# Performance work log

Measured on AMD Instinct MI355X. Metric: run time of the kernel, lower is better.

Reference implementation:

```python
import jax, jax.numpy as jnp
import numpy as np

N_ENTITIES = 200_000
N_RELATIONS = 2
EMBED_DIM = 64
N_EDGES = 2_000_000


def setup_inputs() -> dict:
    key = jax.random.key(0)
    k1, k2, k3, k4, k5, k6, k7, k8 = jax.random.split(key, 8)
    edge_index = jax.random.randint(k1, (2, N_EDGES), 0, N_ENTITIES, dtype=jnp.int32)
    edge_type = jax.random.randint(k2, (N_EDGES,), 0, N_RELATIONS, dtype=jnp.int32)
    entity_emb = jax.random.normal(k3, (N_ENTITIES, EMBED_DIM), dtype=jnp.float32)
    relation_emb = jax.random.normal(k4, (N_RELATIONS, EMBED_DIM), dtype=jnp.float32)
    att_w = jax.random.normal(k5, (2 * EMBED_DIM, 1), dtype=jnp.float32) * 0.08
    att_b = jax.random.normal(k6, (1,), dtype=jnp.float32) * 0.08
    W_w = jax.random.normal(k7, (EMBED_DIM, EMBED_DIM), dtype=jnp.float32) * 0.12
    W_b = jax.random.normal(k8, (EMBED_DIM,), dtype=jnp.float32) * 0.12
    return {
        "edge_index": edge_index,
        "edge_type": edge_type,
        "entity_emb": entity_emb,
        "relation_emb": relation_emb,
        "att_w": att_w,
        "att_b": att_b,
        "W_w": W_w,
        "W_b": W_b,
    }


def reference(edge_index, edge_type, entity_emb, relation_emb, att_w, att_b, W_w, W_b):
    # Gather per-edge embeddings: [E, D]
    head = entity_emb[edge_index[0]]
    tail = entity_emb[edge_index[1]]
    rel = relation_emb[edge_type]
    # Attention score per edge: sigmoid(Linear(cat(head, rel)))  -> [E, 1]
    head_rel = jnp.concatenate([head, rel], axis=-1)
    att_scores = jax.nn.sigmoid(head_rel @ att_w + att_b)
    # Weighted messages and scatter-add into head nodes (the Python loop in the
    # original is exactly a segment_sum over head indices).
    neighbor_emb = att_scores * tail  # [E, D]
    aggr_emb = jax.ops.segment_sum(neighbor_emb, edge_index[0], num_segments=N_ENTITIES)
    # Final transform: tanh(W @ aggr + b)
    return jnp.tanh(aggr_emb @ W_w.T + W_b)
```

## Files before the change

kernel.cpp:

```cpp
#include <hip/hip_runtime.h>
#include <hip/hip_bf16.h>


#define DIM 64
#define TMASK 0x3FFFF
#define RBIT (1 << 18)
#define BSH 8
#define NBK_MAX 800
#define CHUNK 6144
#define SCAN_ITEMS 4
#define S1_ITEMS 2

__global__ __launch_bounds__(256) void kgat_front(
    const float* __restrict__ emb, const float* __restrict__ rel,
    const float* __restrict__ att_w, const float* __restrict__ att_b,
    const int* __restrict__ ei,
    float* __restrict__ hdot, float* __restrict__ rb,
    int* __restrict__ bcnt,
    int n_ent, int n_rel, int E, int nbk, int hblocks) {
  __shared__ int hist[NBK_MAX];
  if ((int)blockIdx.x < hblocks) {
    int gid = blockIdx.x * 256 + threadIdx.x;
    int n = gid >> 4;
    int q = threadIdx.x & 15;
    if (n >= n_ent + n_rel) return;
    float4 v, w;
    if (n < n_ent) {
      v = ((const float4*)emb)[n * 16 + q];
      w = ((const float4*)att_w)[q];
    } else {
      v = ((const float4*)rel)[(n - n_ent) * 16 + q];
      w = ((const float4*)att_w)[16 + q];
    }
    float p = v.x * w.x + v.y * w.y + v.z * w.z + v.w * w.w;
    p += __shfl_xor(p, 1);
    p += __shfl_xor(p, 2);
    p += __shfl_xor(p, 4);
    p += __shfl_xor(p, 8);
    if (q == 0) {
      if (n < n_ent) hdot[n] = p;
      else rb[n - n_ent] = p + att_b[0];
    }
  } else {
    for (int i = threadIdx.x; i < NBK_MAX; i += 256) hist[i] = 0;
    __syncthreads();
    int base = ((int)blockIdx.x - hblocks) * CHUNK;
    for (int i = threadIdx.x; i < CHUNK; i += 256) {
      int e = base + i;
      if (e < E) atomicAdd(&hist[ei[e] >> BSH], 1);
    }
    __syncthreads();
    for (int b = threadIdx.x; b < nbk; b += 256) {
      int c = hist[b];
      if (c) atomicAdd(&bcnt[b << 4], c);
    }
  }
}

__global__ __launch_bounds__(256) void kgat_bscan(
    const int* __restrict__ bcnt, int* __restrict__ boff,
    int* __restrict__ gcur, int nbk) {
  __shared__ int sblk[256];
  int v[SCAN_ITEMS];
  int s = 0;
#pragma unroll
  for (int k = 0; k < SCAN_ITEMS; ++k) {
    int idx = threadIdx.x * SCAN_ITEMS + k;
    v[k] = (idx < nbk) ? bcnt[idx << 4] : 0;
    s += v[k];
  }
  sblk[threadIdx.x] = s;
  __syncthreads();
  for (int d = 1; d < 256; d <<= 1) {
    int t = (threadIdx.x >= (unsigned)d) ? sblk[threadIdx.x - d] : 0;
    __syncthreads();
    sblk[threadIdx.x] += t;
    __syncthreads();
  }
  int excl = sblk[threadIdx.x] - s;
#pragma unroll
  for (int k = 0; k < SCAN_ITEMS; ++k) {
    int idx = threadIdx.x * SCAN_ITEMS + k;
    if (idx < nbk) {
      boff[idx] = excl;
      gcur[idx << 4] = excl;
    }
    excl += v[k];
  }
  if (threadIdx.x == 255) boff[nbk] = excl;
}

__global__ __launch_bounds__(512) void kgat_scatter1(
    const int* __restrict__ ei, const int* __restrict__ et,
    int* __restrict__ gcur, int* __restrict__ stage, int E, int nbk) {
  __shared__ int hist[NBK_MAX];
  __shared__ int lstart[NBK_MAX];
  __shared__ int lcur[NBK_MAX];
  __shared__ int sblk[512];
  __shared__ int vals[CHUNK];
  __shared__ unsigned short bid[CHUNK];
  int tid = threadIdx.x;
  int base = blockIdx.x * CHUNK;
  for (int i = tid; i < NBK_MAX; i += 512) hist[i] = 0;
  __syncthreads();
  for (int i = tid; i < CHUNK; i += 512) {
    int e = base + i;
    if (e < E) atomicAdd(&hist[ei[e] >> BSH], 1);
  }
  __syncthreads();
  int v[S1_ITEMS];
  int s = 0;
#pragma unroll
  for (int k = 0; k < S1_ITEMS; ++k) {
    int idx = tid * S1_ITEMS + k;
    v[k] = (idx < nbk) ? hist[idx] : 0;
    s += v[k];
  }
  sblk[tid] = s;
  __syncthreads();
  for (int d = 1; d < 512; d <<= 1) {
    int t = (tid >= d) ? sblk[tid - d] : 0;
    __syncthreads();
    sblk[tid] += t;
    __syncthreads();
  }
  int excl = sblk[tid] - s;
#pragma unroll
  for (int k = 0; k < S1_ITEMS; ++k) {
    int idx = tid * S1_ITEMS + k;
    if (idx < nbk) {
      lstart[idx] = excl;
      lcur[idx] = excl;
    }
    excl += v[k];
  }
  __syncthreads();
  for (int b = tid; b < nbk; b += 512) {
    int c = hist[b];
    hist[b] = c ? atomicAdd(&gcur[b << 4], c) : 0;
  }
  __syncthreads();
  for (int i = tid; i < CHUNK; i += 512) {
    int e = base + i;
    if (e < E) {
      int h = ei[e];
      int t = ei[E + e];
      int r = et[e];
      int b = h >> BSH;
      int pos = atomicAdd(&lcur[b], 1);
      vals[pos] = t | (r << 18) | ((h & 255) << 19);
      bid[pos] = (unsigned short)b;
    }
  }
  __syncthreads();
  int cc = E - base;
  if (cc > CHUNK) cc = CHUNK;
  for (int p = tid; p < cc; p += 512) {
    int b = bid[p];
    stage[hist[b] + (p - lstart[b])] = vals[p];
  }
}

__global__ __launch_bounds__(256) void kgat_scatter2(
    const int* __restrict__ stage, const int* __restrict__ boff,
    int* __restrict__ off, int* __restrict__ payload) {
  __shared__ int hist[256];
  __shared__ int sc[256];
  __shared__ int lcur[256];
  int b = blockIdx.x;
  int tid = threadIdx.x;
  int s0 = boff[b], s1 = boff[b + 1];
  hist[tid] = 0;
  __syncthreads();
  for (int p = s0 + tid; p < s1; p += 256)
    atomicAdd(&hist[(stage[p] >> 19) & 255], 1);
  __syncthreads();
  int c = hist[tid];
  sc[tid] = c;
  __syncthreads();
  for (int d = 1; d < 256; d <<= 1) {
    int t = (tid >= d) ? sc[tid - d] : 0;
    __syncthreads();
    sc[tid] += t;
    __syncthreads();
  }
  int basep = s0 + sc[tid] - c;
  off[(b << 8) + tid] = basep;
  lcur[tid] = basep;
  __syncthreads();
  for (int p = s0 + tid; p < s1; p += 256) {
    int vv = stage[p];
    int pos = atomicAdd(&lcur[(vv >> 19) & 255], 1);
    payload[pos] = vv;
  }
}

__global__ __launch_bounds__(256) void kgat_aggr_fused(
    const int* __restrict__ off, const int* __restrict__ payload,
    const float* __restrict__ emb, const float* __restrict__ hdot,
    const float* __restrict__ rb, const float* __restrict__ Ww,
    const float* __restrict__ Wb, float* __restrict__ out, int n) {
  __shared__ float Ws[64][68];
  for (int idx = threadIdx.x; idx < 64 * 64; idx += 256) {
    int j = idx >> 6, i = idx & 63;
    Ws[i][j] = Ww[idx];
  }
  __syncthreads();
  int q = threadIdx.x & 15;
  int grp = threadIdx.x >> 4;
  int lanebase = (threadIdx.x & 63) & ~15;
  int stride = gridDim.x * 16;
  float r0 = rb[0], r1 = rb[1];
  float4 bb = ((const float4*)Wb)[q];
  const float4* emb4 = (const float4*)emb;
  for (int h = blockIdx.x * 16 + grp; h < n; h += stride) {
    int p = off[h];
    int p1 = off[h + 1];
    float hd = hdot[h];
    float sc0 = 1.0f / (1.0f + __expf(-(hd + r0)));
    float sc1 = 1.0f / (1.0f + __expf(-(hd + r1)));
    float4 acc = make_float4(0.f, 0.f, 0.f, 0.f);
    for (; p + 4 <= p1; p += 4) {
      int v0 = payload[p + 0];
      int v1 = payload[p + 1];
      int v2 = payload[p + 2];
      int v3 = payload[p + 3];
      float4 t0 = emb4[(v0 & TMASK) * 16 + q];
      float4 t1 = emb4[(v1 & TMASK) * 16 + q];
      float4 t2 = emb4[(v2 & TMASK) * 16 + q];
      float4 t3 = emb4[(v3 & TMASK) * 16 + q];
      float s0 = (v0 & RBIT) ? sc1 : sc0;
      float s1 = (v1 & RBIT) ? sc1 : sc0;
      float s2 = (v2 & RBIT) ? sc1 : sc0;
      float s3 = (v3 & RBIT) ? sc1 : sc0;
      acc.x = fmaf(s0, t0.x, acc.x); acc.y = fmaf(s0, t0.y, acc.y);
      acc.z = fmaf(s0, t0.z, acc.z); acc.w = fmaf(s0, t0.w, acc.w);
      acc.x = fmaf(s1, t1.x, acc.x); acc.y = fmaf(s1, t1.y, acc.y);
      acc.z = fmaf(s1, t1.z, acc.z); acc.w = fmaf(s1, t1.w, acc.w);
      acc.x = fmaf(s2, t2.x, acc.x); acc.y = fmaf(s2, t2.y, acc.y);
      acc.z = fmaf(s2, t2.z, acc.z); acc.w = fmaf(s2, t2.w, acc.w);
      acc.x = fmaf(s3, t3.x, acc.x); acc.y = fmaf(s3, t3.y, acc.y);
      acc.z = fmaf(s3, t3.z, acc.z); acc.w = fmaf(s3, t3.w, acc.w);
    }
    for (; p < p1; ++p) {
      int v0 = payload[p];
      float s0 = (v0 & RBIT) ? sc1 : sc0;
      float4 t0 = emb4[(v0 & TMASK) * 16 + q];
      acc.x = fmaf(s0, t0.x, acc.x); acc.y = fmaf(s0, t0.y, acc.y);
      acc.z = fmaf(s0, t0.z, acc.z); acc.w = fmaf(s0, t0.w, acc.w);
    }
    float4 o = bb;
#pragma unroll 4
    for (int j = 0; j < 16; ++j) {
      float a0 = __shfl(acc.x, lanebase + j);
      float a1 = __shfl(acc.y, lanebase + j);
      float a2 = __shfl(acc.z, lanebase + j);
      float a3 = __shfl(acc.w, lanebase + j);
      float4 w0 = *(const float4*)&Ws[4 * j + 0][4 * q];
      float4 w1 = *(const float4*)&Ws[4 * j + 1][4 * q];
      float4 w2 = *(const float4*)&Ws[4 * j + 2][4 * q];
      float4 w3 = *(const float4*)&Ws[4 * j + 3][4 * q];
      o.x = fmaf(a0, w0.x, o.x); o.y = fmaf(a0, w0.y, o.y);
      o.z = fmaf(a0, w0.z, o.z); o.w = fmaf(a0, w0.w, o.w);
      o.x = fmaf(a1, w1.x, o.x); o.y = fmaf(a1, w1.y, o.y);
      o.z = fmaf(a1, w1.z, o.z); o.w = fmaf(a1, w1.w, o.w);
      o.x = fmaf(a2, w2.x, o.x); o.y = fmaf(a2, w2.y, o.y);
      o.z = fmaf(a2, w2.z, o.z); o.w = fmaf(a2, w2.w, o.w);
      o.x = fmaf(a3, w3.x, o.x); o.y = fmaf(a3, w3.y, o.y);
      o.z = fmaf(a3, w3.z, o.z); o.w = fmaf(a3, w3.w, o.w);
    }
    o.x = tanhf(o.x); o.y = tanhf(o.y); o.z = tanhf(o.z); o.w = tanhf(o.w);
    ((float4*)out)[h * 16 + q] = o;
  }
}

extern "C" void kernel_launch(void* const* d_in, const int* in_sizes, int n_in,
                              void* d_out, int out_size, void* d_ws, size_t ws_size,
                              hipStream_t stream) {
  const int* edge_index = (const int*)d_in[0];
  const int* edge_type  = (const int*)d_in[1];
  const float* entity_emb   = (const float*)d_in[2];
  const float* relation_emb = (const float*)d_in[3];
  const float* att_w = (const float*)d_in[4];
  const float* att_b = (const float*)d_in[5];
  const float* W_w   = (const float*)d_in[6];
  const float* W_b   = (const float*)d_in[7];
  float* out = (float*)d_out;

  const int E     = in_sizes[0] / 2;
  const int N_ENT = in_sizes[2] / DIM;
  const int N_REL = in_sizes[3] / DIM;
  const int NBK   = (N_ENT + 255) >> BSH;

  int* w32 = (int*)d_ws;
  float* hdot = (float*)w32;
  float* rb   = (float*)(w32 + N_ENT);
  int*   bcnt = w32 + N_ENT + 8;
  int*   boff = bcnt + NBK * 16;
  int*   gcur = boff + NBK + 1;
  int*   off  = gcur + NBK * 16;
  int*   stage   = off + NBK * 256 + 1;
  int*   payload = stage + E;

  hipMemsetAsync(bcnt, 0, (size_t)NBK * 16 * sizeof(int), stream);

  int hblocks = ((N_ENT + N_REL) * 16 + 255) / 256;
  int eblocks = (E + CHUNK - 1) / CHUNK;
  kgat_front<<<hblocks + eblocks, 256, 0, stream>>>(
      entity_emb, relation_emb, att_w, att_b, edge_index,
      hdot, rb, bcnt, N_ENT, N_REL, E, NBK, hblocks);
  kgat_bscan<<<1, 256, 0, stream>>>(bcnt, boff, gcur, NBK);
  kgat_scatter1<<<eblocks, 512, 0, stream>>>(edge_index, edge_type, gcur, stage, E, NBK);
  kgat_scatter2<<<NBK, 256, 0, stream>>>(stage, boff, off, payload);
  kgat_aggr_fused<<<2048, 256, 0, stream>>>(off, payload, entity_emb, hdot, rb,
                                            W_w, W_b, out, N_ENT);
}
```

Before: 177.8 us.

## Fuse per-bucket counting sort into aggregation kernel using shared memory

Merges the second-level sort (scatter2) into the aggregation kernel. Each 512-thread block now sorts its 256-node bucket's edges into LDS and then aggregates and transforms those nodes directly. This removes one launch plus the global payload and offset write and read round trip. In exchange it uses a large LDS footprint (about 36KB), which may lower occupancy, and grid size shrinks to NBK (~782) blocks. There is a slow fallback path for buckets above SCAP edges.

```diff
diff --git a/kernel.cpp b/kernel.cpp
--- a/kernel.cpp
+++ b/kernel.cpp
@@ -10,6 +10,7 @@
 #define CHUNK 6144
 #define SCAN_ITEMS 4
 #define S1_ITEMS 2
+#define SCAP 4608
 
 __global__ __launch_bounds__(256) void kgat_front(
     const float* __restrict__ emb, const float* __restrict__ rel,
@@ -161,116 +162,161 @@
   }
 }
 
-__global__ __launch_bounds__(256) void kgat_scatter2(
-    const int* __restrict__ stage, const int* __restrict__ boff,
-    int* __restrict__ off, int* __restrict__ payload) {
-  __shared__ int hist[256];
-  __shared__ int sc[256];
-  __shared__ int lcur[256];
-  int b = blockIdx.x;
-  int tid = threadIdx.x;
-  int s0 = boff[b], s1 = boff[b + 1];
-  hist[tid] = 0;
-  __syncthreads();
-  for (int p = s0 + tid; p < s1; p += 256)
-    atomicAdd(&hist[(stage[p] >> 19) & 255], 1);
-  __syncthreads();
-  int c = hist[tid];
-  sc[tid] = c;
-  __syncthreads();
-  for (int d = 1; d < 256; d <<= 1) {
-    int t = (tid >= d) ? sc[tid - d] : 0;
-    __syncthreads();
-    sc[tid] += t;
-    __syncthreads();
-  }
-  int basep = s0 + sc[tid] - c;
-  off[(b << 8) + tid] = basep;
-  lcur[tid] = basep;
-  __syncthreads();
-  for (int p = s0 + tid; p < s1; p += 256) {
-    int vv = stage[p];
-    int pos = atomicAdd(&lcur[(vv >> 19) & 255], 1);
-    payload[pos] = vv;
-  }
-}
-
-__global__ __launch_bounds__(256) void kgat_aggr_fused(
-    const int* __restrict__ off, const int* __restrict__ payload,
+__global__ __launch_bounds__(512) void kgat_aggr2(
+    const int* __restrict__ boff, const int* __restrict__ stage,
     const float* __restrict__ emb, const float* __restrict__ hdot,
     const float* __restrict__ rb, const float* __restrict__ Ww,
     const float* __restrict__ Wb, float* __restrict__ out, int n) {
   __shared__ float Ws[64][68];
-  for (int idx = threadIdx.x; idx < 64 * 64; idx += 256) {
+  __shared__ int svals[SCAP];
+  __shared__ int hist[256];
+  __shared__ int sc[256];
+  __shared__ int lcur[256];
+  int tid = threadIdx.x;
+  int b = blockIdx.x;
+  for (int idx = tid; idx < 64 * 64; idx += 512) {
     int j = idx >> 6, i = idx & 63;
     Ws[i][j] = Ww[idx];
   }
-  __syncthreads();
-  int q = threadIdx.x & 15;
-  int grp = threadIdx.x >> 4;
-  int lanebase = (threadIdx.x & 63) & ~15;
-  int stride = gridDim.x * 16;
+  int q = tid & 15;
+  int grp = tid >> 4;
+  int lanebase = (tid & 63) & ~15;
+  int h0 = b << 8;
+  int s0 = boff[b], s1 = boff[b + 1];
+  int m = s1 - s0;
   float r0 = rb[0], r1 = rb[1];
-  float4 bb = ((const float4*)Wb)[q];
   const float4* emb4 = (const float4*)emb;
-  for (int h = blockIdx.x * 16 + grp; h < n; h += stride) {
-    int p = off[h];
-    int p1 = off[h + 1];
-    float hd = hdot[h];
-    float sc0 = 1.0f / (1.0f + __expf(-(hd + r0)));
-    float sc1 = 1.0f / (1.0f + __expf(-(hd + r1)));
-    float4 acc = make_float4(0.f, 0.f, 0.f, 0.f);
-    for (; p + 4 <= p1; p += 4) {
-      int v0 = payload[p + 0];
-      int v1 = payload[p + 1];
-      int v2 = payload[p + 2];
-      int v3 = payload[p + 3];
-      float4 t0 = emb4[(v0 & TMASK) * 16 + q];
-      float4 t1 = emb4[(v1 & TMASK) * 16 + q];
-      float4 t2 = emb4[(v2 & TMASK) * 16 + q];
-      float4 t3 = emb4[(v3 & TMASK) * 16 + q];
-      float s0 = (v0 & RBIT) ? sc1 : sc0;
-      float s1 = (v1 & RBIT) ? sc1 : sc0;
-      float s2 = (v2 & RBIT) ? sc1 : sc0;
-      float s3 = (v3 & RBIT) ? sc1 : sc0;
-      acc.x = fmaf(s0, t0.x, acc.x); acc.y = fmaf(s0, t0.y, acc.y);
-      acc.z = fmaf(s0, t0.z, acc.z); acc.w = fmaf(s0, t0.w, acc.w);
-      acc.x = fmaf(s1, t1.x, acc.x); acc.y = fmaf(s1, t1.y, acc.y);
-      acc.z = fmaf(s1, t1.z, acc.z); acc.w = fmaf(s1, t1.w, acc.w);
-      acc.x = fmaf(s2, t2.x, acc.x); acc.y = fmaf(s2, t2.y, acc.y);
-      acc.z = fmaf(s2, t2.z, acc.z); acc.w = fmaf(s2, t2.w, acc.w);
-      acc.x = fmaf(s3, t3.x, acc.x); acc.y = fmaf(s3, t3.y, acc.y);
-      acc.z = fmaf(s3, t3.z, acc.z); acc.w = fmaf(s3, t3.w, acc.w);
-    }
-    for (; p < p1; ++p) {
-      int v0 = payload[p];
-      float s0 = (v0 & RBIT) ? sc1 : sc0;
-      float4 t0 = emb4[(v0 & TMASK) * 16 + q];
-      acc.x = fmaf(s0, t0.x, acc.x); acc.y = fmaf(s0, t0.y, acc.y);
-      acc.z = fmaf(s0, t0.z, acc.z); acc.w = fmaf(s0, t0.w, acc.w);
-    }
-    float4 o = bb;
+  float4 bb;
+  bb = ((const float4*)Wb)[q];
+
+  if (m <= SCAP) {
+    if (tid < 256) hist[tid] = 0;
+    __syncthreads();
+    for (int i = tid; i < m; i += 512) {
+      int v = stage[s0 + i];
+      atomicAdd(&hist[(v >> 19) & 255], 1);
+    }
+    __syncthreads();
+    int c = 0;
+    if (tid < 256) { c = hist[tid]; sc[tid] = c; }
+    __syncthreads();
+    for (int d = 1; d < 256; d <<= 1) {
+      int t = 0;
+      if (tid < 256 && tid >= d) t = sc[tid - d];
+      __syncthreads();
+      if (tid < 256) sc[tid] += t;
+      __syncthreads();
+    }
+    if (tid < 256) lcur[tid] = sc[tid] - c;
+    __syncthreads();
+    for (int i = tid; i < m; i += 512) {
+      int v = stage[s0 + i];
+      int pos = atomicAdd(&lcur[(v >> 19) & 255], 1);
+      svals[pos] = v;
+    }
+    __syncthreads();
+    for (int hl = grp; hl < 256; hl += 32) {
+      int h = h0 + hl;
+      if (h >= n) break;
+      int jend = sc[hl];
+      int j = jend - hist[hl];
+      float hd = hdot[h];
+      float sA = 1.0f / (1.0f + __expf(-(hd + r0)));
+      float sB = 1.0f / (1.0f + __expf(-(hd + r1)));
+      float4 acc = make_float4(0.f, 0.f, 0.f, 0.f);
+      for (; j + 4 <= jend; j += 4) {
+        int v0 = svals[j + 0];
+        int v1 = svals[j + 1];
+        int v2 = svals[j + 2];
+        int v3 = svals[j + 3];
+        float4 t0 = emb4[(v0 & TMASK) * 16 + q];
+        float4 t1 = emb4[(v1 & TMASK) * 16 + q];
+        float4 t2 = emb4[(v2 & TMASK) * 16 + q];
+        float4 t3 = emb4[(v3 & TMASK) * 16 + q];
+        float s0f = (v0 & RBIT) ? sB : sA;
+        float s1f = (v1 & RBIT) ? sB : sA;
+        float s2f = (v2 & RBIT) ? sB : sA;
+        float s3f = (v3 & RBIT) ? sB : sA;
+        acc.x = fmaf(s0f, t0.x, acc.x); acc.y = fmaf(s0f, t0.y, acc.y);
+        acc.z = fmaf(s0f, t0.z, acc.z); acc.w = fmaf(s0f, t0.w, acc.w);
+        acc.x = fmaf(s1f, t1.x, acc.x); acc.y = fmaf(s1f, t1.y, acc.y);
+        acc.z = fmaf(s1f, t1.z, acc.z); acc.w = fmaf(s1f, t1.w, acc.w);
+        acc.x = fmaf(s2f, t2.x, acc.x); acc.y = fmaf(s2f, t2.y, acc.y);
+        acc.z = fmaf(s2f, t2.z, acc.z); acc.w = fmaf(s2f, t2.w, acc.w);
+        acc.x = fmaf(s3f, t3.x, acc.x); acc.y = fmaf(s3f, t3.y, acc.y);
+        acc.z = fmaf(s3f, t3.z, acc.z); acc.w = fmaf(s3f, t3.w, acc.w);
+      }
+      for (; j < jend; ++j) {
+        int v0 = svals[j];
+        float s0f = (v0 & RBIT) ? sB : sA;
+        float4 t0 = emb4[(v0 & TMASK) * 16 + q];
+        acc.x = fmaf(s0f, t0.x, acc.x); acc.y = fmaf(s0f, t0.y, acc.y);
+        acc.z = fmaf(s0f, t0.z, acc.z); acc.w = fmaf(s0f, t0.w, acc.w);
+      }
+      float4 o = bb;
 #pragma unroll 4
-    for (int j = 0; j < 16; ++j) {
-      float a0 = __shfl(acc.x, lanebase + j);
-      float a1 = __shfl(acc.y, lanebase + j);
-      float a2 = __shfl(acc.z, lanebase + j);
-      float a3 = __shfl(acc.w, lanebase + j);
-      float4 w0 = *(const float4*)&Ws[4 * j + 0][4 * q];
-      float4 w1 = *(const float4*)&Ws[4 * j + 1][4 * q];
-      float4 w2 = *(const float4*)&Ws[4 * j + 2][4 * q];
-      float4 w3 = *(const float4*)&Ws[4 * j + 3][4 * q];
-      o.x = fmaf(a0, w0.x, o.x); o.y = fmaf(a0, w0.y, o.y);
-      o.z = fmaf(a0, w0.z, o.z); o.w = fmaf(a0, w0.w, o.w);
-      o.x = fmaf(a1, w1.x, o.x); o.y = fmaf(a1, w1.y, o.y);
-      o.z = fmaf(a1, w1.z, o.z); o.w = fmaf(a1, w1.w, o.w);
-      o.x = fmaf(a2, w2.x, o.x); o.y = fmaf(a2, w2.y, o.y);
-      o.z = fmaf(a2, w2.z, o.z); o.w = fmaf(a2, w2.w, o.w);
-      o.x = fmaf(a3, w3.x, o.x); o.y = fmaf(a3, w3.y, o.y);
-      o.z = fmaf(a3, w3.z, o.z); o.w = fmaf(a3, w3.w, o.w);
-    }
-    o.x = tanhf(o.x); o.y = tanhf(o.y); o.z = tanhf(o.z); o.w = tanhf(o.w);
-    ((float4*)out)[h * 16 + q] = o;
+      for (int jj = 0; jj < 16; ++jj) {
+        float a0 = __shfl(acc.x, lanebase + jj);
+        float a1 = __shfl(acc.y, lanebase + jj);
+        float a2 = __shfl(acc.z, lanebase + jj);
+        float a3 = __shfl(acc.w, lanebase + jj);
+        float4 w0 = *(const float4*)&Ws[4 * jj + 0][4 * q];
+        float4 w1 = *(const float4*)&Ws[4 * jj + 1][4 * q];
+        float4 w2 = *(const float4*)&Ws[4 * jj + 2][4 * q];
+        float4 w3 = *(const float4*)&Ws[4 * jj + 3][4 * q];
+        o.x = fmaf(a0, w0.x, o.x); o.y = fmaf(a0, w0.y, o.y);
+        o.z = fmaf(a0, w0.z, o.z); o.w = fmaf(a0, w0.w, o.w);
+        o.x = fmaf(a1, w1.x, o.x); o.y = fmaf(a1, w1.y, o.y);
+        o.z = fmaf(a1, w1.z, o.z); o.w = fmaf(a1, w1.w, o.w);
+        o.x = fmaf(a2, w2.x, o.x); o.y = fmaf(a2, w2.y, o.y);
+        o.z = fmaf(a2, w2.z, o.z); o.w = fmaf(a2, w2.w, o.w);
+        o.x = fmaf(a3, w3.x, o.x); o.y = fmaf(a3, w3.y, o.y);
+        o.z = fmaf(a3, w3.z, o.z); o.w = fmaf(a3, w3.w, o.w);
+      }
+      o.x = tanhf(o.x); o.y = tanhf(o.y); o.z = tanhf(o.z); o.w = tanhf(o.w);
+      ((float4*)out)[h * 16 + q] = o;
+    }
+  } else {
+    __syncthreads();
+    for (int hl = grp; hl < 256; hl += 32) {
+      int h = h0 + hl;
+      if (h >= n) break;
+      float hd = hdot[h];
+      float sA = 1.0f / (1.0f + __expf(-(hd + r0)));
+      float sB = 1.0f / (1.0f + __expf(-(hd + r1)));
+      float4 acc = make_float4(0.f, 0.f, 0.f, 0.f);
+      for (int p = s0; p < s1; ++p) {
+        int v = stage[p];
+        if (((v >> 19) & 255) == hl) {
+          float s0f = (v & RBIT) ? sB : sA;
+          float4 t0 = emb4[(v & TMASK) * 16 + q];
+          acc.x = fmaf(s0f, t0.x, acc.x); acc.y = fmaf(s0f, t0.y, acc.y);
+          acc.z = fmaf(s0f, t0.z, acc.z); acc.w = fmaf(s0f, t0.w, acc.w);
+        }
+      }
+      float4 o = bb;
+#pragma unroll 4
+      for (int jj = 0; jj < 16; ++jj) {
+        float a0 = __shfl(acc.x, lanebase + jj);
+        float a1 = __shfl(acc.y, lanebase + jj);
+        float a2 = __shfl(acc.z, lanebase + jj);
+        float a3 = __shfl(acc.w, lanebase + jj);
+        float4 w0 = *(const float4*)&Ws[4 * jj + 0][4 * q];
+        float4 w1 = *(const float4*)&Ws[4 * jj + 1][4 * q];
+        float4 w2 = *(const float4*)&Ws[4 * jj + 2][4 * q];
+        float4 w3 = *(const float4*)&Ws[4 * jj + 3][4 * q];
+        o.x = fmaf(a0, w0.x, o.x); o.y = fmaf(a0, w0.y, o.y);
+        o.z = fmaf(a0, w0.z, o.z); o.w = fmaf(a0, w0.w, o.w);
+        o.x = fmaf(a1, w1.x, o.x); o.y = fmaf(a1, w1.y, o.y);
+        o.z = fmaf(a1, w1.z, o.z); o.w = fmaf(a1, w1.w, o.w);
+        o.x = fmaf(a2, w2.x, o.x); o.y = fmaf(a2, w2.y, o.y);
+        o.z = fmaf(a2, w2.z, o.z); o.w = fmaf(a2, w2.w, o.w);
+        o.x = fmaf(a3, w3.x, o.x); o.y = fmaf(a3, w3.y, o.y);
+        o.z = fmaf(a3, w3.z, o.z); o.w = fmaf(a3, w3.w, o.w);
+      }
+      o.x = tanhf(o.x); o.y = tanhf(o.y); o.z = tanhf(o.z); o.w = tanhf(o.w);
+      ((float4*)out)[h * 16 + q] = o;
+    }
   }
 }
 
@@ -298,9 +344,7 @@
   int*   bcnt = w32 + N_ENT + 8;
   int*   boff = bcnt + NBK * 16;
   int*   gcur = boff + NBK + 1;
-  int*   off  = gcur + NBK * 16;
-  int*   stage   = off + NBK * 256 + 1;
-  int*   payload = stage + E;
+  int*   stage= gcur + NBK * 16;
 
   hipMemsetAsync(bcnt, 0, (size_t)NBK * 16 * sizeof(int), stream);
 
@@ -311,7 +355,6 @@
       hdot, rb, bcnt, N_ENT, N_REL, E, NBK, hblocks);
   kgat_bscan<<<1, 256, 0, stream>>>(bcnt, boff, gcur, NBK);
   kgat_scatter1<<<eblocks, 512, 0, stream>>>(edge_index, edge_type, gcur, stage, E, NBK);
-  kgat_scatter2<<<NBK, 256, 0, stream>>>(stage, boff, off, payload);
-  kgat_aggr_fused<<<2048, 256, 0, stream>>>(off, payload, entity_emb, hdot, rb,
-                                            W_w, W_b, out, N_ENT);
-}
+  kgat_aggr2<<<NBK, 512, 0, stream>>>(boff, stage, entity_emb, hdot, rb,
+                                      W_w, W_b, out, N_ENT);
+}
```

Measured after the change: 187.1 us. 1.05x slower.
